# Kernel optimization log

Hardware: AMD Instinct MI355X
Metric: run time of the kernel (lower is better)

The kernel has to match this reference:

```python
import jax, jax.numpy as jnp
import numpy as np

E = 8            # num_experts
DIM = 2880       # model dim
HID = 2880       # expert hidden dim (mlp1 outputs 2*HID, interleaved glu/linear)
T = 16384        # total dispatched tokens, evenly split across experts
SWIGLU_LIMIT = 7.0
ALPHA = 1.702


def swiglu(x, alpha=ALPHA, limit=SWIGLU_LIMIT):
    # interleaved: even channels -> glu gate, odd channels -> linear
    x_glu = x[..., ::2]
    x_lin = x[..., 1::2]
    x_glu = jnp.minimum(x_glu, limit)
    x_lin = jnp.clip(x_lin, -limit, limit)
    return x_glu * jax.nn.sigmoid(alpha * x_glu) * (x_lin + 1.0)


def setup_inputs() -> dict:
    key = jax.random.key(0)
    k1, k2, k3, k4, k5 = jax.random.split(key, 5)
    scale = 0.02
    x = jax.random.normal(k1, (T, DIM), dtype=jnp.float32)
    num_tokens_per_expert = jnp.full((E,), T // E, dtype=jnp.int64)
    mlp1_weight = jax.random.normal(k2, (E, 2 * HID, DIM), dtype=jnp.float32) * scale
    mlp1_bias = jax.random.normal(k3, (E, 2 * HID), dtype=jnp.float32) * scale
    mlp2_weight = jax.random.normal(k4, (E, DIM, HID), dtype=jnp.float32) * scale
    mlp2_bias = jax.random.normal(k5, (E, DIM), dtype=jnp.float32) * scale
    return {
        "x": x,
        "num_tokens_per_expert": num_tokens_per_expert,
        "mlp1_weight": mlp1_weight,
        "mlp1_bias": mlp1_bias,
        "mlp2_weight": mlp2_weight,
        "mlp2_bias": mlp2_bias,
    }


def reference(x, num_tokens_per_expert, mlp1_weight, mlp1_bias, mlp2_weight, mlp2_bias):
    # Equal token counts per expert (as constructed): grouped GEMM == batched GEMM
    # over a reshaped [E, T/E, DIM] view. tp_degree == 1 so ScaleBiasForward is identity.
    tpe = T // E
    xg = x.reshape(E, tpe, DIM)                                  # [E, t, D]
    h = jnp.einsum("etd,ehd->eth", xg, mlp1_weight)              # [E, t, 2H]
    h = h + mlp1_bias[:, None, :]
    h = swiglu(h)                                                # [E, t, H]
    out = jnp.einsum("eth,edh->etd", h, mlp2_weight)             # [E, t, D]
    out = out + mlp2_bias[:, None, :]
    return out.reshape(T, DIM)
```

## Files before the change

kernel.cpp:

```cpp
#include <hip/hip_runtime.h>
#include <hip/hip_bf16.h>


#define TT   16384
#define DIM_ 2880
#define HID_ 2880
#define NE   8
#define TPE  2048
#define KDIM 2880
#define NT   45

typedef __attribute__((ext_vector_type(8))) short short8;
typedef __attribute__((ext_vector_type(4))) float f32x4;

__device__ __forceinline__ unsigned short f2bf(float f) {
  unsigned u = __builtin_bit_cast(unsigned, f);
  u += 0x7fffu + ((u >> 16) & 1u);
  return (unsigned short)(u >> 16);
}

__global__ void __launch_bounds__(256) cvt_f32_bf16(const float* __restrict__ src,
                                                    unsigned short* __restrict__ dst,
                                                    long n) {
  long i = ((long)blockIdx.x * 256 + threadIdx.x) * 8;
  if (i >= n) return;
  float4 a = *(const float4*)(src + i);
  float4 b = *(const float4*)(src + i + 4);
  union { unsigned short u[8]; short8 v; } r;
  r.u[0] = f2bf(a.x); r.u[1] = f2bf(a.y); r.u[2] = f2bf(a.z); r.u[3] = f2bf(a.w);
  r.u[4] = f2bf(b.x); r.u[5] = f2bf(b.y); r.u[6] = f2bf(b.z); r.u[7] = f2bf(b.w);
  *(short8*)(dst + i) = r.v;
}

#define GLDS(gsrc, ldst) \
  __builtin_amdgcn_global_load_lds( \
      (const __attribute__((address_space(1))) unsigned int*)(gsrc), \
      (__attribute__((address_space(3))) unsigned int*)(ldst), 16, 0, 0)

template<bool FUSE_SWIGLU>
__global__ void __launch_bounds__(512, 2) gemm8(const unsigned short* __restrict__ A,
                                                const unsigned short* __restrict__ B,
                                                const float* __restrict__ bias,
                                                void* __restrict__ Cout,
                                                int M, int N) {
  __shared__ unsigned short As[2][256 * 64];
  __shared__ unsigned short Bs[2][320 * 64];

  const int tid  = threadIdx.x;
  const int lane = tid & 63;
  const int wid  = tid >> 6;
  const int wr   = wid >> 2;
  const int wc   = wid & 3;
  const int e    = blockIdx.z;

  const int ntn   = N / 320;
  const int ntm   = M / 256;
  const int per_e = ntn * ntm;
  const int bid   = blockIdx.x;
  const int swz   = (bid & 7) * (per_e >> 3) + (bid >> 3);
  const int m0    = (swz / ntn) * 256;
  const int n0    = (swz % ntn) * 320;

  const int srow = tid >> 3;
  const int scol = ((tid & 7) ^ (srow & 7)) << 3;
  const unsigned short* Aexp = A + ((size_t)e * M + m0 + srow) * KDIM + scol;
  const unsigned short* Bexp = B + ((size_t)e * N + n0 + srow) * KDIM + scol;

  auto stage = [&](int buf, int kt) {
    const unsigned short* asrc = Aexp + (size_t)kt * 64;
#pragma unroll
    for (int j = 0; j < 4; ++j)
      GLDS(asrc + (size_t)(j * 64) * KDIM, &As[buf][j * 4096 + tid * 8]);
    const unsigned short* bsrc = Bexp + (size_t)kt * 64;
#pragma unroll
    for (int j = 0; j < 5; ++j)
      GLDS(bsrc + (size_t)(j * 64) * KDIM, &Bs[buf][j * 4096 + tid * 8]);
  };

  const int arow = (wr * 128 + (lane & 15)) * 128;
  const int brow = (wc * 80  + (lane & 15)) * 128;
  const int swzb = (lane & 7) << 4;
  const int kb   = ((lane >> 4) & 3) * 16;
  const int c0 = kb ^ swzb;
  const int c1 = (64 + kb) ^ swzb;

  f32x4 acc[8][5] = {};

  stage(0, 0);
  stage(1, 1);
  asm volatile("s_waitcnt vmcnt(9)" ::: "memory");
  __builtin_amdgcn_s_barrier();

  for (int t = 0; t < NT; ++t) {
    const int cur = t & 1;
    const char* aB = (const char*)(&As[cur][0]) + arow;
    const char* bB = (const char*)(&Bs[cur][0]) + brow;

    short8 a0[8], a1[8], b0[5], b1[5];
#pragma unroll
    for (int fm = 0; fm < 8; ++fm) {
      a0[fm] = *(const short8*)(aB + fm * 2048 + c0);
      a1[fm] = *(const short8*)(aB + fm * 2048 + c1);
    }
#pragma unroll
    for (int fn = 0; fn < 5; ++fn) {
      b0[fn] = *(const short8*)(bB + fn * 2048 + c0);
      b1[fn] = *(const short8*)(bB + fn * 2048 + c1);
    }

#pragma unroll
    for (int fn = 0; fn < 5; ++fn)
#pragma unroll
      for (int fm = 0; fm < 8; ++fm)
        acc[fm][fn] = __builtin_amdgcn_mfma_f32_16x16x32_bf16(a0[fm], b0[fn], acc[fm][fn], 0, 0, 0);

    asm volatile("s_waitcnt lgkmcnt(0)" ::: "memory");
    __builtin_amdgcn_s_barrier();

    const bool more = (t + 2 < NT);
    if (more) stage(cur, t + 2);

    __builtin_amdgcn_s_setprio(1);
#pragma unroll
    for (int fn = 0; fn < 5; ++fn)
#pragma unroll
      for (int fm = 0; fm < 8; ++fm)
        acc[fm][fn] = __builtin_amdgcn_mfma_f32_16x16x32_bf16(a1[fm], b1[fn], acc[fm][fn], 0, 0, 0);
    __builtin_amdgcn_s_setprio(0);

    if (more) asm volatile("s_waitcnt vmcnt(9)" ::: "memory");
    else      asm volatile("s_waitcnt vmcnt(0)" ::: "memory");
    __builtin_amdgcn_s_barrier();
  }

  const float* be = bias + (size_t)e * N;
  if constexpr (FUSE_SWIGLU) {
    unsigned short* ha = (unsigned short*)Cout + (size_t)e * M * (N >> 1);
#pragma unroll
    for (int fm = 0; fm < 8; ++fm)
#pragma unroll
      for (int fn = 0; fn < 5; ++fn) {
        const int col = n0 + wc * 80 + fn * 16 + (lane & 15);
        const float bc = be[col];
#pragma unroll
        for (int j = 0; j < 4; ++j) {
          const int row = m0 + wr * 128 + fm * 16 + (lane >> 4) * 4 + j;
          float v = acc[fm][fn][j] + bc;
          float p = __shfl_xor(v, 1);
          if (!(lane & 1)) {
            float g  = fminf(v, 7.0f);
            float l2 = fminf(fmaxf(p, -7.0f), 7.0f);
            float act = g / (1.0f + __expf(-1.702f * g)) * (l2 + 1.0f);
            ha[(size_t)row * (N >> 1) + (col >> 1)] = f2bf(act);
          }
        }
      }
  } else {
    float* out = (float*)Cout + (size_t)e * M * N;
#pragma unroll
    for (int fm = 0; fm < 8; ++fm)
#pragma unroll
      for (int fn = 0; fn < 5; ++fn) {
        const int col = n0 + wc * 80 + fn * 16 + (lane & 15);
        const float bc = be[col];
#pragma unroll
        for (int j = 0; j < 4; ++j) {
          const int row = m0 + wr * 128 + fm * 16 + (lane >> 4) * 4 + j;
          out[(size_t)row * N + col] = acc[fm][fn][j] + bc;
        }
      }
  }
}

extern "C" void kernel_launch(void* const* d_in, const int* in_sizes, int n_in,
                              void* d_out, int out_size, void* d_ws, size_t ws_size,
                              hipStream_t stream) {
  const float* x  = (const float*)d_in[0];
  const float* w1 = (const float*)d_in[2];
  const float* b1 = (const float*)d_in[3];
  const float* w2 = (const float*)d_in[4];
  const float* b2 = (const float*)d_in[5];

  unsigned short* xb  = (unsigned short*)d_ws;
  unsigned short* w1b = xb  + (size_t)TT * DIM_;
  unsigned short* w2b = w1b + (size_t)NE * 2 * HID_ * DIM_;
  unsigned short* ha  = w2b + (size_t)NE * DIM_ * HID_;

  const long nx = (long)TT * DIM_;
  const long n1 = (long)NE * 2 * HID_ * DIM_;
  const long n2 = (long)NE * DIM_ * HID_;
  cvt_f32_bf16<<<(int)(nx / 2048), 256, 0, stream>>>(x,  xb,  nx);
  cvt_f32_bf16<<<(int)(n1 / 2048), 256, 0, stream>>>(w1, w1b, n1);
  cvt_f32_bf16<<<(int)(n2 / 2048), 256, 0, stream>>>(w2, w2b, n2);

  dim3 g1((5760 / 320) * (TPE / 256), 1, NE);
  gemm8<true><<<g1, 512, 0, stream>>>(xb, w1b, b1, ha, TPE, 5760);

  dim3 g2((DIM_ / 320) * (TPE / 256), 1, NE);
  gemm8<false><<<g2, 512, 0, stream>>>(ha, w2b, b2, (float*)d_out, TPE, DIM_);
}
```

Before: 1.178 ms.

## Widen GEMM1 N-tile, restructure k-loop, fuse w2 conversion into GEMM1 epilogue

Templates the GEMM on the N fragment count so GEMM1 uses 384-wide tiles (6 fragments) while GEMM2 keeps 320. The k-loop now loads and multiplies each half of the tile in turn with fewer live registers, and waits for all outstanding loads before issuing the next stage instead of overlapping it with the second MFMA half. The separate w2 fp32-to-bf16 conversion kernel is folded into the tail of GEMM1 as a grid-stride loop. The aim is better operand reuse and one fewer launch, at the risk of weaker load/compute overlap and a larger LDS footprint per block.

```diff
diff --git a/kernel.cpp b/kernel.cpp
--- a/kernel.cpp
+++ b/kernel.cpp
@@ -37,14 +37,18 @@
       (const __attribute__((address_space(1))) unsigned int*)(gsrc), \
       (__attribute__((address_space(3))) unsigned int*)(ldst), 16, 0, 0)
 
-template<bool FUSE_SWIGLU>
-__global__ void __launch_bounds__(512, 2) gemm8(const unsigned short* __restrict__ A,
+template<int FN, bool FUSE_SWIGLU>
+__global__ void __launch_bounds__(512, 2) gemmk(const unsigned short* __restrict__ A,
                                                 const unsigned short* __restrict__ B,
                                                 const float* __restrict__ bias,
                                                 void* __restrict__ Cout,
-                                                int M, int N) {
+                                                int M, int N,
+                                                const float* __restrict__ cvt_src,
+                                                unsigned short* __restrict__ cvt_dst,
+                                                long cvt_n) {
+  constexpr int BN = 64 * FN;
   __shared__ unsigned short As[2][256 * 64];
-  __shared__ unsigned short Bs[2][320 * 64];
+  __shared__ unsigned short Bs[2][BN * 64];
 
   const int tid  = threadIdx.x;
   const int lane = tid & 63;
@@ -53,13 +57,13 @@
   const int wc   = wid & 3;
   const int e    = blockIdx.z;
 
-  const int ntn   = N / 320;
+  const int ntn   = N / BN;
   const int ntm   = M / 256;
   const int per_e = ntn * ntm;
   const int bid   = blockIdx.x;
   const int swz   = (bid & 7) * (per_e >> 3) + (bid >> 3);
   const int m0    = (swz / ntn) * 256;
-  const int n0    = (swz % ntn) * 320;
+  const int n0    = (swz % ntn) * BN;
 
   const int srow = tid >> 3;
   const int scol = ((tid & 7) ^ (srow & 7)) << 3;
@@ -73,22 +77,23 @@
       GLDS(asrc + (size_t)(j * 64) * KDIM, &As[buf][j * 4096 + tid * 8]);
     const unsigned short* bsrc = Bexp + (size_t)kt * 64;
 #pragma unroll
-    for (int j = 0; j < 5; ++j)
+    for (int j = 0; j < FN; ++j)
       GLDS(bsrc + (size_t)(j * 64) * KDIM, &Bs[buf][j * 4096 + tid * 8]);
   };
 
   const int arow = (wr * 128 + (lane & 15)) * 128;
-  const int brow = (wc * 80  + (lane & 15)) * 128;
+  const int brow = (wc * (FN * 16) + (lane & 15)) * 128;
   const int swzb = (lane & 7) << 4;
   const int kb   = ((lane >> 4) & 3) * 16;
   const int c0 = kb ^ swzb;
   const int c1 = (64 + kb) ^ swzb;
 
-  f32x4 acc[8][5] = {};
+  f32x4 acc[8][FN] = {};
 
   stage(0, 0);
   stage(1, 1);
-  asm volatile("s_waitcnt vmcnt(9)" ::: "memory");
+  if constexpr (FN == 6) asm volatile("s_waitcnt vmcnt(10)" ::: "memory");
+  else                   asm volatile("s_waitcnt vmcnt(9)"  ::: "memory");
   __builtin_amdgcn_s_barrier();
 
   for (int t = 0; t < NT; ++t) {
@@ -96,41 +101,36 @@
     const char* aB = (const char*)(&As[cur][0]) + arow;
     const char* bB = (const char*)(&Bs[cur][0]) + brow;
 
-    short8 a0[8], a1[8], b0[5], b1[5];
-#pragma unroll
-    for (int fm = 0; fm < 8; ++fm) {
-      a0[fm] = *(const short8*)(aB + fm * 2048 + c0);
-      a1[fm] = *(const short8*)(aB + fm * 2048 + c1);
-    }
-#pragma unroll
-    for (int fn = 0; fn < 5; ++fn) {
-      b0[fn] = *(const short8*)(bB + fn * 2048 + c0);
-      b1[fn] = *(const short8*)(bB + fn * 2048 + c1);
-    }
-
-#pragma unroll
-    for (int fn = 0; fn < 5; ++fn)
+    short8 a[8], b[FN];
+
+#pragma unroll
+    for (int fm = 0; fm < 8; ++fm) a[fm] = *(const short8*)(aB + fm * 2048 + c0);
+#pragma unroll
+    for (int fn = 0; fn < FN; ++fn) b[fn] = *(const short8*)(bB + fn * 2048 + c0);
+    __builtin_amdgcn_s_setprio(1);
+#pragma unroll
+    for (int fn = 0; fn < FN; ++fn)
 #pragma unroll
       for (int fm = 0; fm < 8; ++fm)
-        acc[fm][fn] = __builtin_amdgcn_mfma_f32_16x16x32_bf16(a0[fm], b0[fn], acc[fm][fn], 0, 0, 0);
+        acc[fm][fn] = __builtin_amdgcn_mfma_f32_16x16x32_bf16(a[fm], b[fn], acc[fm][fn], 0, 0, 0);
+    __builtin_amdgcn_s_setprio(0);
+
+#pragma unroll
+    for (int fm = 0; fm < 8; ++fm) a[fm] = *(const short8*)(aB + fm * 2048 + c1);
+#pragma unroll
+    for (int fn = 0; fn < FN; ++fn) b[fn] = *(const short8*)(bB + fn * 2048 + c1);
+    __builtin_amdgcn_s_setprio(1);
+#pragma unroll
+    for (int fn = 0; fn < FN; ++fn)
+#pragma unroll
+      for (int fm = 0; fm < 8; ++fm)
+        acc[fm][fn] = __builtin_amdgcn_mfma_f32_16x16x32_bf16(a[fm], b[fn], acc[fm][fn], 0, 0, 0);
+    __builtin_amdgcn_s_setprio(0);
 
     asm volatile("s_waitcnt lgkmcnt(0)" ::: "memory");
+    asm volatile("s_waitcnt vmcnt(0)" ::: "memory");
     __builtin_amdgcn_s_barrier();
-
-    const bool more = (t + 2 < NT);
-    if (more) stage(cur, t + 2);
-
-    __builtin_amdgcn_s_setprio(1);
-#pragma unroll
-    for (int fn = 0; fn < 5; ++fn)
-#pragma unroll
-      for (int fm = 0; fm < 8; ++fm)
-        acc[fm][fn] = __builtin_amdgcn_mfma_f32_16x16x32_bf16(a1[fm], b1[fn], acc[fm][fn], 0, 0, 0);
-    __builtin_amdgcn_s_setprio(0);
-
-    if (more) asm volatile("s_waitcnt vmcnt(9)" ::: "memory");
-    else      asm volatile("s_waitcnt vmcnt(0)" ::: "memory");
-    __builtin_amdgcn_s_barrier();
+    if (t + 2 < NT) stage(cur, t + 2);
   }
 
   const float* be = bias + (size_t)e * N;
@@ -139,8 +139,8 @@
 #pragma unroll
     for (int fm = 0; fm < 8; ++fm)
 #pragma unroll
-      for (int fn = 0; fn < 5; ++fn) {
-        const int col = n0 + wc * 80 + fn * 16 + (lane & 15);
+      for (int fn = 0; fn < FN; ++fn) {
+        const int col = n0 + wc * (FN * 16) + fn * 16 + (lane & 15);
         const float bc = be[col];
 #pragma unroll
         for (int j = 0; j < 4; ++j) {
@@ -155,13 +155,23 @@
           }
         }
       }
+    const long stride = (long)gridDim.x * gridDim.z * 512 * 8;
+    long i = ((long)(blockIdx.z * gridDim.x + blockIdx.x) * 512 + tid) * 8;
+    for (; i < cvt_n; i += stride) {
+      float4 va = *(const float4*)(cvt_src + i);
+      float4 vb = *(const float4*)(cvt_src + i + 4);
+      union { unsigned short u[8]; short8 v; } r;
+      r.u[0] = f2bf(va.x); r.u[1] = f2bf(va.y); r.u[2] = f2bf(va.z); r.u[3] = f2bf(va.w);
+      r.u[4] = f2bf(vb.x); r.u[5] = f2bf(vb.y); r.u[6] = f2bf(vb.z); r.u[7] = f2bf(vb.w);
+      *(short8*)(cvt_dst + i) = r.v;
+    }
   } else {
     float* out = (float*)Cout + (size_t)e * M * N;
 #pragma unroll
     for (int fm = 0; fm < 8; ++fm)
 #pragma unroll
-      for (int fn = 0; fn < 5; ++fn) {
-        const int col = n0 + wc * 80 + fn * 16 + (lane & 15);
+      for (int fn = 0; fn < FN; ++fn) {
+        const int col = n0 + wc * (FN * 16) + fn * 16 + (lane & 15);
         const float bc = be[col];
 #pragma unroll
         for (int j = 0; j < 4; ++j) {
@@ -191,11 +201,11 @@
   const long n2 = (long)NE * DIM_ * HID_;
   cvt_f32_bf16<<<(int)(nx / 2048), 256, 0, stream>>>(x,  xb,  nx);
   cvt_f32_bf16<<<(int)(n1 / 2048), 256, 0, stream>>>(w1, w1b, n1);
-  cvt_f32_bf16<<<(int)(n2 / 2048), 256, 0, stream>>>(w2, w2b, n2);
-
-  dim3 g1((5760 / 320) * (TPE / 256), 1, NE);
-  gemm8<true><<<g1, 512, 0, stream>>>(xb, w1b, b1, ha, TPE, 5760);
-
-  dim3 g2((DIM_ / 320) * (TPE / 256), 1, NE);
-  gemm8<false><<<g2, 512, 0, stream>>>(ha, w2b, b2, (float*)d_out, TPE, DIM_);
-}
+
+  dim3 g1(5760 / 384 * (TPE / 256), 1, NE);
+  gemmk<6, true><<<g1, 512, 0, stream>>>(xb, w1b, b1, ha, TPE, 5760, w2, w2b, n2);
+
+  dim3 g2(DIM_ / 320 * (TPE / 256), 1, NE);
+  gemmk<5, false><<<g2, 512, 0, stream>>>(ha, w2b, b2, (float*)d_out, TPE, DIM_,
+                                          nullptr, nullptr, 0);
+}
```

Result: slower. 1.272 ms (+8.0%).

## Rewrite first expert GEMM as 256x256 tile with four-phase interleaved load/MFMA schedule

Applied to the files above, without the earlier changes.

Adds a dedicated kernel for the first GEMM that uses 256x256 tiles instead of 256x320 and pads the N edge with clamped loads and masked stores. Its K-loop is split into four phases that interleave partial LDS fragment reads, half-tile global-to-LDS prefetches and MFMA batches, so memory traffic overlaps compute more finely. The aim is better latency hiding and a smaller register footprint per wave. In exchange it needs more barriers per K step and wastes work on the padded final N tile, since 5760 is not a multiple of 256. The second GEMM is unchanged apart from dropping the template.

```diff
diff --git a/kernel.cpp b/kernel.cpp
--- a/kernel.cpp
+++ b/kernel.cpp
@@ -9,6 +9,8 @@
 #define TPE  2048
 #define KDIM 2880
 #define NT   45
+#define NB1  5760
+#define NT1P 23
 
 typedef __attribute__((ext_vector_type(8))) short short8;
 typedef __attribute__((ext_vector_type(4))) float f32x4;
@@ -37,12 +39,183 @@
       (const __attribute__((address_space(1))) unsigned int*)(gsrc), \
       (__attribute__((address_space(3))) unsigned int*)(ldst), 16, 0, 0)
 
-template<bool FUSE_SWIGLU>
-__global__ void __launch_bounds__(512, 2) gemm8(const unsigned short* __restrict__ A,
-                                                const unsigned short* __restrict__ B,
-                                                const float* __restrict__ bias,
-                                                void* __restrict__ Cout,
-                                                int M, int N) {
+#define MFMA(a, b, c) __builtin_amdgcn_mfma_f32_16x16x32_bf16(a, b, c, 0, 0, 0)
+
+__global__ void __launch_bounds__(512, 2) gemm1_8ph(const unsigned short* __restrict__ A,
+                                                    const unsigned short* __restrict__ B,
+                                                    const float* __restrict__ bias,
+                                                    unsigned short* __restrict__ ha) {
+  __shared__ unsigned short As[2][256 * 64];
+  __shared__ unsigned short Bs[2][256 * 64];
+
+  const int tid  = threadIdx.x;
+  const int lane = tid & 63;
+  const int wid  = tid >> 6;
+  const int wr   = wid >> 2;
+  const int wc   = wid & 3;
+  const int e    = blockIdx.z;
+
+  const int per_e = 8 * NT1P;
+  const int bid   = blockIdx.x;
+  const int swz   = (bid & 7) * (per_e >> 3) + (bid >> 3);
+  const int m0    = (swz / NT1P) * 256;
+  const int n0    = (swz % NT1P) * 256;
+
+  const unsigned short* Ae = A + (size_t)e * TPE * KDIM;
+  const unsigned short* Be = B + (size_t)e * NB1 * KDIM;
+
+  const int srow0 = (wid << 4) + (lane >> 3);
+
+  auto stA = [&](int buf, int kt, int h) {
+#pragma unroll
+    for (int i = 0; i < 2; ++i) {
+      const int row = srow0 + i * 8;
+      const int sc  = ((lane & 7) ^ (row & 7)) << 3;
+      GLDS(Ae + (size_t)(m0 + h * 128 + row) * KDIM + kt * 64 + sc,
+           &As[buf][h * 8192 + ((wid << 4) + i * 8) * 64 + lane * 8]);
+    }
+  };
+  auto stB = [&](int buf, int kt, int h) {
+#pragma unroll
+    for (int i = 0; i < 2; ++i) {
+      const int row = srow0 + i * 8;
+      int gr = n0 + h * 128 + row;
+      gr = gr < NB1 ? gr : NB1 - 1;
+      const int sc = ((lane & 7) ^ (row & 7)) << 3;
+      GLDS(Be + (size_t)gr * KDIM + kt * 64 + sc,
+           &Bs[buf][h * 8192 + ((wid << 4) + i * 8) * 64 + lane * 8]);
+    }
+  };
+
+  const int arow = wr * 16384 + (lane & 15) * 128;
+  const int brow = (wc >> 1) * 16384 + ((wc & 1) * 64 + (lane & 15)) * 128;
+  const int swzb = (lane & 7) << 4;
+  const int kb   = ((lane >> 4) & 3) * 16;
+  const int c0 = kb ^ swzb;
+  const int c1 = (64 + kb) ^ swzb;
+
+  f32x4 acc[8][4] = {};
+
+  stB(0, 0, 0); stA(0, 0, 0); stB(0, 0, 1); stA(0, 0, 1);
+  stB(1, 1, 0); stA(1, 1, 0);
+  asm volatile("s_waitcnt vmcnt(4)" ::: "memory");
+  __builtin_amdgcn_s_barrier();
+
+  for (int t = 0; t < NT; ++t) {
+    const int cur = t & 1;
+    const char* aB = (const char*)&As[cur][0] + arow;
+    const char* bB = (const char*)&Bs[cur][0] + brow;
+    const bool s1 = (t + 1 < NT), s2 = (t + 2 < NT);
+
+    short8 a0[4], a1[4], b0[4], b1[4];
+
+#pragma unroll
+    for (int i = 0; i < 4; ++i) {
+      a0[i] = *(const short8*)(aB + i * 2048 + c0);
+      a1[i] = *(const short8*)(aB + i * 2048 + c1);
+    }
+#pragma unroll
+    for (int f = 0; f < 2; ++f) {
+      b0[f] = *(const short8*)(bB + f * 2048 + c0);
+      b1[f] = *(const short8*)(bB + f * 2048 + c1);
+    }
+    if (s1) stB(cur ^ 1, t + 1, 1);
+    asm volatile("s_waitcnt lgkmcnt(8)" ::: "memory");
+    __builtin_amdgcn_s_barrier();
+    asm volatile("s_waitcnt lgkmcnt(0)" ::: "memory");
+    __builtin_amdgcn_s_setprio(1);
+#pragma unroll
+    for (int f = 0; f < 2; ++f)
+#pragma unroll
+      for (int i = 0; i < 4; ++i) {
+        acc[i][f] = MFMA(a0[i], b0[f], acc[i][f]);
+        acc[i][f] = MFMA(a1[i], b1[f], acc[i][f]);
+      }
+    __builtin_amdgcn_s_setprio(0);
+    __builtin_amdgcn_s_barrier();
+
+#pragma unroll
+    for (int f = 2; f < 4; ++f) {
+      b0[f] = *(const short8*)(bB + f * 2048 + c0);
+      b1[f] = *(const short8*)(bB + f * 2048 + c1);
+    }
+    if (s1) stA(cur ^ 1, t + 1, 1);
+    __builtin_amdgcn_s_barrier();
+    asm volatile("s_waitcnt lgkmcnt(0)" ::: "memory");
+    __builtin_amdgcn_s_setprio(1);
+#pragma unroll
+    for (int f = 2; f < 4; ++f)
+#pragma unroll
+      for (int i = 0; i < 4; ++i) {
+        acc[i][f] = MFMA(a0[i], b0[f], acc[i][f]);
+        acc[i][f] = MFMA(a1[i], b1[f], acc[i][f]);
+      }
+    __builtin_amdgcn_s_setprio(0);
+    __builtin_amdgcn_s_barrier();
+
+#pragma unroll
+    for (int i = 0; i < 4; ++i) {
+      a0[i] = *(const short8*)(aB + (4 + i) * 2048 + c0);
+      a1[i] = *(const short8*)(aB + (4 + i) * 2048 + c1);
+    }
+    if (s2) stB(cur, t + 2, 0);
+    __builtin_amdgcn_s_barrier();
+    asm volatile("s_waitcnt lgkmcnt(0)" ::: "memory");
+    __builtin_amdgcn_s_setprio(1);
+#pragma unroll
+    for (int f = 2; f < 4; ++f)
+#pragma unroll
+      for (int i = 0; i < 4; ++i) {
+        acc[4 + i][f] = MFMA(a0[i], b0[f], acc[4 + i][f]);
+        acc[4 + i][f] = MFMA(a1[i], b1[f], acc[4 + i][f]);
+      }
+    __builtin_amdgcn_s_setprio(0);
+    __builtin_amdgcn_s_barrier();
+
+    if (s2) stA(cur, t + 2, 0);
+    __builtin_amdgcn_s_setprio(1);
+#pragma unroll
+    for (int f = 0; f < 2; ++f)
+#pragma unroll
+      for (int i = 0; i < 4; ++i) {
+        acc[4 + i][f] = MFMA(a0[i], b0[f], acc[4 + i][f]);
+        acc[4 + i][f] = MFMA(a1[i], b1[f], acc[4 + i][f]);
+      }
+    __builtin_amdgcn_s_setprio(0);
+    if (s2) asm volatile("s_waitcnt vmcnt(4)" ::: "memory");
+    else    asm volatile("s_waitcnt vmcnt(0)" ::: "memory");
+    __builtin_amdgcn_s_barrier();
+  }
+
+  const float* be = bias + (size_t)e * NB1;
+  unsigned short* hae = ha + (size_t)e * TPE * HID_;
+#pragma unroll
+  for (int fm = 0; fm < 8; ++fm)
+#pragma unroll
+    for (int fn = 0; fn < 4; ++fn) {
+      const int col = n0 + wc * 64 + fn * 16 + (lane & 15);
+      const bool ok = col < NB1;
+      const float bc = ok ? be[col] : 0.0f;
+#pragma unroll
+      for (int j = 0; j < 4; ++j) {
+        const int row = m0 + wr * 128 + fm * 16 + (lane >> 4) * 4 + j;
+        float v = acc[fm][fn][j] + bc;
+        float p = __shfl_xor(v, 1);
+        if (!(lane & 1) && ok) {
+          float g  = fminf(v, 7.0f);
+          float l2 = fminf(fmaxf(p, -7.0f), 7.0f);
+          float act = g / (1.0f + __expf(-1.702f * g)) * (l2 + 1.0f);
+          hae[(size_t)row * HID_ + (col >> 1)] = f2bf(act);
+        }
+      }
+    }
+}
+
+__global__ void __launch_bounds__(512, 2) gemm2k(const unsigned short* __restrict__ A,
+                                                 const unsigned short* __restrict__ B,
+                                                 const float* __restrict__ bias,
+                                                 float* __restrict__ Cout,
+                                                 int M, int N) {
   __shared__ unsigned short As[2][256 * 64];
   __shared__ unsigned short Bs[2][320 * 64];
 
@@ -112,7 +285,7 @@
     for (int fn = 0; fn < 5; ++fn)
 #pragma unroll
       for (int fm = 0; fm < 8; ++fm)
-        acc[fm][fn] = __builtin_amdgcn_mfma_f32_16x16x32_bf16(a0[fm], b0[fn], acc[fm][fn], 0, 0, 0);
+        acc[fm][fn] = MFMA(a0[fm], b0[fn], acc[fm][fn]);
 
     asm volatile("s_waitcnt lgkmcnt(0)" ::: "memory");
     __builtin_amdgcn_s_barrier();
@@ -125,7 +298,7 @@
     for (int fn = 0; fn < 5; ++fn)
 #pragma unroll
       for (int fm = 0; fm < 8; ++fm)
-        acc[fm][fn] = __builtin_amdgcn_mfma_f32_16x16x32_bf16(a1[fm], b1[fn], acc[fm][fn], 0, 0, 0);
+        acc[fm][fn] = MFMA(a1[fm], b1[fn], acc[fm][fn]);
     __builtin_amdgcn_s_setprio(0);
 
     if (more) asm volatile("s_waitcnt vmcnt(9)" ::: "memory");
@@ -134,42 +307,19 @@
   }
 
   const float* be = bias + (size_t)e * N;
-  if constexpr (FUSE_SWIGLU) {
-    unsigned short* ha = (unsigned short*)Cout + (size_t)e * M * (N >> 1);
-#pragma unroll
-    for (int fm = 0; fm < 8; ++fm)
-#pragma unroll
-      for (int fn = 0; fn < 5; ++fn) {
-        const int col = n0 + wc * 80 + fn * 16 + (lane & 15);
-        const float bc = be[col];
-#pragma unroll
-        for (int j = 0; j < 4; ++j) {
-          const int row = m0 + wr * 128 + fm * 16 + (lane >> 4) * 4 + j;
-          float v = acc[fm][fn][j] + bc;
-          float p = __shfl_xor(v, 1);
-          if (!(lane & 1)) {
-            float g  = fminf(v, 7.0f);
-            float l2 = fminf(fmaxf(p, -7.0f), 7.0f);
-            float act = g / (1.0f + __expf(-1.702f * g)) * (l2 + 1.0f);
-            ha[(size_t)row * (N >> 1) + (col >> 1)] = f2bf(act);
-          }
-        }
-      }
-  } else {
-    float* out = (float*)Cout + (size_t)e * M * N;
-#pragma unroll
-    for (int fm = 0; fm < 8; ++fm)
-#pragma unroll
-      for (int fn = 0; fn < 5; ++fn) {
-        const int col = n0 + wc * 80 + fn * 16 + (lane & 15);
-        const float bc = be[col];
-#pragma unroll
-        for (int j = 0; j < 4; ++j) {
-          const int row = m0 + wr * 128 + fm * 16 + (lane >> 4) * 4 + j;
-          out[(size_t)row * N + col] = acc[fm][fn][j] + bc;
-        }
-      }
-  }
+  float* out = Cout + (size_t)e * (size_t)M * N;
+#pragma unroll
+  for (int fm = 0; fm < 8; ++fm)
+#pragma unroll
+    for (int fn = 0; fn < 5; ++fn) {
+      const int col = n0 + wc * 80 + fn * 16 + (lane & 15);
+      const float bc = be[col];
+#pragma unroll
+      for (int j = 0; j < 4; ++j) {
+        const int row = m0 + wr * 128 + fm * 16 + (lane >> 4) * 4 + j;
+        out[(size_t)row * N + col] = acc[fm][fn][j] + bc;
+      }
+    }
 }
 
 extern "C" void kernel_launch(void* const* d_in, const int* in_sizes, int n_in,
@@ -193,9 +343,9 @@
   cvt_f32_bf16<<<(int)(n1 / 2048), 256, 0, stream>>>(w1, w1b, n1);
   cvt_f32_bf16<<<(int)(n2 / 2048), 256, 0, stream>>>(w2, w2b, n2);
 
-  dim3 g1((5760 / 320) * (TPE / 256), 1, NE);
-  gemm8<true><<<g1, 512, 0, stream>>>(xb, w1b, b1, ha, TPE, 5760);
+  dim3 g1(8 * NT1P, 1, NE);
+  gemm1_8ph<<<g1, 512, 0, stream>>>(xb, w1b, b1, ha);
 
   dim3 g2((DIM_ / 320) * (TPE / 256), 1, NE);
-  gemm8<false><<<g2, 512, 0, stream>>>(ha, w2b, b2, (float*)d_out, TPE, DIM_);
-}
+  gemm2k<<<g2, 512, 0, stream>>>(ha, w2b, b2, (float*)d_out, TPE, DIM_);
+}
```

Result: slower. 1.330 ms (+12.9%).
